# Kernel optimization log

Measured on AMD Instinct MI355X. Metric: run time of the kernel, lower is better.

## Reference

```python
import jax, jax.numpy as jnp
import numpy as np

B, S, E, H = 2, 2048, 1024, 16
D = E // H  # 64 head dim


def _rope_tables(seq_len, d_head, base=10000.0):
    half = d_head // 2
    inv_freq = 1.0 / (base ** (np.arange(0, half, dtype=np.float32) / half))
    t = np.arange(seq_len, dtype=np.float32)
    ang = np.outer(t, inv_freq)  # [S, d_head/2]
    return jnp.asarray(np.cos(ang)), jnp.asarray(np.sin(ang))


def setup_inputs() -> dict:
    key = jax.random.key(0)
    k1, k2, k3 = jax.random.split(key, 3)
    x = jax.random.normal(k1, (B, S, E), dtype=jnp.float32)
    w_qkv = jax.random.normal(k2, (E, 3 * E), dtype=jnp.float32) / np.sqrt(E)
    w_out = jax.random.normal(k3, (E, E), dtype=jnp.float32) / np.sqrt(E)
    freqs_cos, freqs_sin = _rope_tables(S, D)
    return {"x": x, "w_qkv": w_qkv, "w_out": w_out,
            "freqs_cos": freqs_cos, "freqs_sin": freqs_sin}


def _apply_rope(x, cos, sin):
    # x: [B, H, S, D]; cos/sin: [S, D/2] -> broadcast [1, 1, S, D/2]
    xr = x.reshape(*x.shape[:-1], D // 2, 2)
    x0, x1 = xr[..., 0], xr[..., 1]
    c = cos[None, None, :, :]
    s = sin[None, None, :, :]
    out = jnp.stack([x0 * c - x1 * s, x0 * s + x1 * c], axis=-1)
    return out.reshape(x.shape)


def reference(x, w_qkv, w_out, freqs_cos, freqs_sin):
    qkv = x @ w_qkv  # [B, S, 3E]
    q, k, v = jnp.split(qkv, 3, axis=-1)
    def heads(t):
        return t.reshape(B, S, H, D).transpose(0, 2, 1, 3)  # [B, H, S, D]
    q, k, v = heads(q), heads(k), heads(v)
    q = _apply_rope(q, freqs_cos, freqs_sin)
    k = _apply_rope(k, freqs_cos, freqs_sin)
    scale = 1.0 / np.sqrt(D).astype(np.float32)
    scores = jnp.einsum('bhsd,bhtd->bhst', q, k) * scale  # [B, H, S, S]
    causal = jnp.tril(jnp.ones((S, S), dtype=bool))
    scores = jnp.where(causal[None, None], scores, jnp.finfo(scores.dtype).min)
    attn = jax.nn.softmax(scores, axis=-1)
    out = jnp.einsum('bhst,bhtd->bhsd', attn, v)  # [B, H, S, D]
    out = out.transpose(0, 2, 1, 3).reshape(B, S, E)
    return out @ w_out  # dropout is identity in eval mode
```

## Files before the change

### kernel.cpp

```cpp
#include <hip/hip_runtime.h>
#include <cstdint>
#include <cstddef>

typedef unsigned short u16;
typedef __attribute__((ext_vector_type(8))) short bf16x8;
typedef __attribute__((ext_vector_type(8))) unsigned short u16x8;
typedef __attribute__((ext_vector_type(4))) float f32x4;

static constexpr int Bc = 2, Sc = 2048, Ec = 1024, Hc = 16, Dc = 64;

__device__ __forceinline__ float bf2f(u16 v) {
    unsigned u = ((unsigned)v) << 16;
    float f; __builtin_memcpy(&f, &u, 4); return f;
}
__device__ __forceinline__ u16 f2bf(float f) {
    unsigned u; __builtin_memcpy(&u, &f, 4);
    u += 0x7fffu + ((u >> 16) & 1u);
    return (u16)(u >> 16);
}
__device__ __forceinline__ bf16x8 as_bf(u16x8 v) { return __builtin_bit_cast(bf16x8, v); }

__global__ void cast_f32_bf16(const float* __restrict__ in, u16* __restrict__ out, int n) {
    int i = (blockIdx.x * blockDim.x + threadIdx.x) * 4;
    if (i < n) {
        float4 v = *reinterpret_cast<const float4*>(in + i);
        ushort4 o;
        o.x = f2bf(v.x); o.y = f2bf(v.y); o.z = f2bf(v.z); o.w = f2bf(v.w);
        *reinterpret_cast<ushort4*>(out + i) = o;
    }
}

__global__ void transpose_cast(const float* __restrict__ in, u16* __restrict__ out,
                               int R, int C) {
    __shared__ float tile[32][33];
    int tx = threadIdx.x, ty = threadIdx.y;
    int c0 = blockIdx.x * 32, r0 = blockIdx.y * 32;
    tile[ty][tx] = in[(size_t)(r0 + ty) * C + c0 + tx];
    __syncthreads();
    out[(size_t)(c0 + ty) * R + r0 + tx] = f2bf(tile[tx][ty]);
}

template <int OUT_BF16>
__global__ __launch_bounds__(256) void gemm_bt(const u16* __restrict__ A,
                                               const u16* __restrict__ Bt,
                                               void* __restrict__ Cout,
                                               int M, int N, int K) {
    constexpr int BK = 32;
    __shared__ u16 As[128][BK];
    __shared__ u16 Bs[128][BK];
    const int m0 = blockIdx.x * 128, n0 = blockIdx.y * 128;
    const int t = threadIdx.x;
    const int lane = t & 63, w = t >> 6;
    const int wr = w >> 1, wc = w & 1;
    const int l15 = lane & 15, lhi = lane >> 4;
    const int lrow = lane >> 2, lcol = (lane & 3) * 8;

    f32x4 acc[4][4] = {};

    for (int k0 = 0; k0 < K; k0 += BK) {
#pragma unroll
        for (int i = 0; i < 2; i++) {
            const u16* ap = A + (size_t)(m0 + w * 32 + i * 16 + lrow) * K + k0 + lcol;
            __builtin_amdgcn_global_load_lds(
                (const __attribute__((address_space(1))) unsigned int*)ap,
                (__attribute__((address_space(3))) unsigned int*)&As[w * 32 + i * 16][0],
                16, 0, 0);
            const u16* bp = Bt + (size_t)(n0 + w * 32 + i * 16 + lrow) * K + k0 + lcol;
            __builtin_amdgcn_global_load_lds(
                (const __attribute__((address_space(1))) unsigned int*)bp,
                (__attribute__((address_space(3))) unsigned int*)&Bs[w * 32 + i * 16][0],
                16, 0, 0);
        }
        __syncthreads();

        bf16x8 af[4], bfv[4];
#pragma unroll
        for (int i = 0; i < 4; i++)
            af[i] = as_bf(*reinterpret_cast<const u16x8*>(&As[wr * 64 + i * 16 + l15][lhi * 8]));
#pragma unroll
        for (int j = 0; j < 4; j++)
            bfv[j] = as_bf(*reinterpret_cast<const u16x8*>(&Bs[wc * 64 + j * 16 + l15][lhi * 8]));
#pragma unroll
        for (int i = 0; i < 4; i++)
#pragma unroll
            for (int j = 0; j < 4; j++)
                acc[i][j] = __builtin_amdgcn_mfma_f32_16x16x32_bf16(af[i], bfv[j], acc[i][j], 0, 0, 0);
        __syncthreads();
    }

#pragma unroll
    for (int i = 0; i < 4; i++)
#pragma unroll
        for (int j = 0; j < 4; j++)
#pragma unroll
            for (int r = 0; r < 4; r++) {
                int row = m0 + wr * 64 + i * 16 + lhi * 4 + r;
                int col = n0 + wc * 64 + j * 16 + l15;
                float v = acc[i][j][r];
                if (OUT_BF16)
                    ((u16*)Cout)[(size_t)row * N + col] = f2bf(v);
                else
                    ((float*)Cout)[(size_t)row * N + col] = v;
            }
}

__global__ void rope_pack(const u16* __restrict__ qkv,
                          const float* __restrict__ fcos, const float* __restrict__ fsin,
                          u16* __restrict__ Qb, u16* __restrict__ Kb) {
    int g = blockIdx.x * blockDim.x + threadIdx.x;
    int dg = g & 3;
    int h = (g >> 2) & 15;
    int row = g >> 6;
    int b = row >> 11, s = row & 2047;
    const float QS = 0.18033688011f;

    const u16* qp = qkv + (size_t)row * 3072 + h * 64 + dg * 16;
    u16x8 q0 = *reinterpret_cast<const u16x8*>(qp);
    u16x8 q1 = *reinterpret_cast<const u16x8*>(qp + 8);
    u16x8 k0 = *reinterpret_cast<const u16x8*>(qp + 1024);
    u16x8 k1 = *reinterpret_cast<const u16x8*>(qp + 1032);

    const float* cp = fcos + (size_t)s * 32 + dg * 8;
    const float* sp = fsin + (size_t)s * 32 + dg * 8;
    float cs[8], sn[8];
#pragma unroll
    for (int p = 0; p < 8; p++) { cs[p] = cp[p]; sn[p] = sp[p]; }

    u16 qi[16], ki[16], qo[16], ko[16];
#pragma unroll
    for (int j = 0; j < 8; j++) { qi[j] = q0[j]; qi[j + 8] = q1[j]; ki[j] = k0[j]; ki[j + 8] = k1[j]; }
#pragma unroll
    for (int p = 0; p < 8; p++) {
        float x0 = bf2f(qi[2 * p]), x1 = bf2f(qi[2 * p + 1]);
        qo[2 * p]     = f2bf((x0 * cs[p] - x1 * sn[p]) * QS);
        qo[2 * p + 1] = f2bf((x0 * sn[p] + x1 * cs[p]) * QS);
        float y0 = bf2f(ki[2 * p]), y1 = bf2f(ki[2 * p + 1]);
        ko[2 * p]     = f2bf(y0 * cs[p] - y1 * sn[p]);
        ko[2 * p + 1] = f2bf(y0 * sn[p] + y1 * cs[p]);
    }

    size_t dst = ((size_t)(b * 16 + h) * 2048 + s) * 64 + dg * 16;
    u16x8 qa, qb2, ka, kb2;
#pragma unroll
    for (int j = 0; j < 8; j++) { qa[j] = qo[j]; qb2[j] = qo[j + 8]; ka[j] = ko[j]; kb2[j] = ko[j + 8]; }
    *reinterpret_cast<u16x8*>(Qb + dst) = qa;
    *reinterpret_cast<u16x8*>(Qb + dst + 8) = qb2;
    *reinterpret_cast<u16x8*>(Kb + dst) = ka;
    *reinterpret_cast<u16x8*>(Kb + dst + 8) = kb2;
}

__global__ __launch_bounds__(256) void vtrans(const u16* __restrict__ qkv,
                                              u16* __restrict__ VT) {
    __shared__ u16 tile[64][70];
    const int bh = blockIdx.y, b = bh >> 4, h = bh & 15;
    const int s0 = blockIdx.x * 64;
    const int t = threadIdx.x;
    const int si = t >> 2, dc = (t & 3) * 16;
    const u16* src = qkv + (size_t)(b * 2048 + s0 + si) * 3072 + 2048 + h * 64 + dc;
    *reinterpret_cast<u16x8*>(&tile[si][dc])     = *reinterpret_cast<const u16x8*>(src);
    *reinterpret_cast<u16x8*>(&tile[si][dc + 8]) = *reinterpret_cast<const u16x8*>(src + 8);
    __syncthreads();
    const int d = t >> 2, sc = (t & 3) * 16;
    u16x8 v0, v1;
#pragma unroll
    for (int j = 0; j < 8; j++) { v0[j] = tile[sc + j][d]; v1[j] = tile[sc + 8 + j][d]; }
    size_t dst = ((size_t)bh * 64 + d) * 2048 + s0 + sc;
    *reinterpret_cast<u16x8*>(VT + dst)     = v0;
    *reinterpret_cast<u16x8*>(VT + dst + 8) = v1;
}

__global__ __launch_bounds__(256) void attn_fwd5(const u16* __restrict__ Qb,
                                                 const u16* __restrict__ Kb,
                                                 const u16* __restrict__ VTb,
                                                 u16* __restrict__ attn_out) {
    __shared__ u16 Ps[4][32 * 70];
    __shared__ float Om[2][32][64];
    __shared__ float Ol[2][32];

    const int t = threadIdx.x, lane = t & 63, w = t >> 6;
    const int l15 = lane & 15, lhi = lane >> 4;
    const int c = w >> 1;
    const int half = w & 1;

    const int id = blockIdx.x;
    const int bh = (id & 7) + 8 * ((id >> 3) & 3);
    const int kk = 31 - (id >> 5);
    const int qc = 2 * kk + c;
    const int q0 = qc * 32;
    const int b = bh >> 4, h = bh & 15;
    const u16* Kp = Kb + (size_t)bh * (Sc * Dc);
    const u16* Vp = VTb + (size_t)bh * (Sc * Dc);
    u16* PsW = &Ps[w][0];

    bf16x8 qf[2][2];
#pragma unroll
    for (int qa = 0; qa < 2; qa++)
#pragma unroll
        for (int kc = 0; kc < 2; kc++)
            qf[qa][kc] = as_bf(*reinterpret_cast<const u16x8*>(
                Qb + (size_t)bh * (Sc * Dc) + (size_t)(q0 + qa * 16 + l15) * 64 + kc * 32 + lhi * 8));

    u16x8 onesu;
#pragma unroll
    for (int j = 0; j < 8; j++) onesu[j] = 0x3F80;
    const bf16x8 onesf = as_bf(onesu);

    f32x4 o[2][4] = {};
    f32x4 os[2] = {};

    const int ntiles = kk + 1;
    const int nh = (ntiles + 1) >> 1;
    const int kt0 = half ? nh : 0;
    const int kt1 = half ? ntiles : nh;
    const int last = (ntiles - 1) * 64;

    for (int kt = kt0; kt < kt1; kt++) {
        const int t0 = kt * 64;

        f32x4 s[2][4];
        {
            bf16x8 kf[4];
#pragma unroll
            for (int cb = 0; cb < 4; cb++)
                kf[cb] = as_bf(*reinterpret_cast<const u16x8*>(
                    Kp + (size_t)(t0 + cb * 16 + l15) * 64 + lhi * 8));
#pragma unroll
            for (int qa = 0; qa < 2; qa++)
#pragma unroll
                for (int cb = 0; cb < 4; cb++) {
                    f32x4 v = {-14.0f, -14.0f, -14.0f, -14.0f};
                    s[qa][cb] = __builtin_amdgcn_mfma_f32_16x16x32_bf16(qf[qa][0], kf[cb], v, 0, 0, 0);
                }
        }
        {
            bf16x8 kf[4];
#pragma unroll
            for (int cb = 0; cb < 4; cb++)
                kf[cb] = as_bf(*reinterpret_cast<const u16x8*>(
                    Kp + (size_t)(t0 + cb * 16 + l15) * 64 + 32 + lhi * 8));
#pragma unroll
            for (int qa = 0; qa < 2; qa++)
#pragma unroll
                for (int cb = 0; cb < 4; cb++)
                    s[qa][cb] = __builtin_amdgcn_mfma_f32_16x16x32_bf16(qf[qa][1], kf[cb], s[qa][cb], 0, 0, 0);
        }

        if (t0 == last) {
#pragma unroll
            for (int qa = 0; qa < 2; qa++)
#pragma unroll
                for (int cb = 0; cb < 4; cb++) {
                    const int tg = t0 + cb * 16 + l15;
#pragma unroll
                    for (int r = 0; r < 4; r++) {
                        const int qg = q0 + qa * 16 + lhi * 4 + r;
                        if (tg > qg) s[qa][cb][r] = -1e30f;
                    }
                }
        }

#pragma unroll
        for (int qa = 0; qa < 2; qa++)
#pragma unroll
            for (int cb = 0; cb < 4; cb++)
#pragma unroll
                for (int r = 0; r < 4; r++) {
                    float p = __builtin_amdgcn_exp2f(s[qa][cb][r]);
                    unsigned pb; __builtin_memcpy(&pb, &p, 4);
                    PsW[(qa * 16 + lhi * 4 + r) * 70 + cb * 16 + l15] = (u16)(pb >> 16);
                }
        asm volatile("s_waitcnt lgkmcnt(0)" ::: "memory");
        __builtin_amdgcn_sched_barrier(0);

#pragma unroll
        for (int kc = 0; kc < 2; kc++) {
            bf16x8 vf[4];
#pragma unroll
            for (int db = 0; db < 4; db++)
                vf[db] = as_bf(*reinterpret_cast<const u16x8*>(
                    Vp + (size_t)(db * 16 + l15) * 2048 + t0 + kc * 32 + lhi * 8));
#pragma unroll
            for (int qa = 0; qa < 2; qa++) {
                bf16x8 pf = as_bf(*reinterpret_cast<const u16x8*>(
                    &PsW[(qa * 16 + l15) * 70 + kc * 32 + lhi * 8]));
                os[qa] = __builtin_amdgcn_mfma_f32_16x16x32_bf16(pf, onesf, os[qa], 0, 0, 0);
#pragma unroll
                for (int db = 0; db < 4; db++)
                    o[qa][db] = __builtin_amdgcn_mfma_f32_16x16x32_bf16(pf, vf[db], o[qa][db], 0, 0, 0);
            }
        }
    }

    if (half) {
#pragma unroll
        for (int qa = 0; qa < 2; qa++)
#pragma unroll
            for (int r = 0; r < 4; r++) {
                const int row = qa * 16 + lhi * 4 + r;
                if (l15 == 0) Ol[c][row] = os[qa][r];
                f32x4 pk;
#pragma unroll
                for (int db = 0; db < 4; db++) pk[db] = o[qa][db][r];
                *reinterpret_cast<f32x4*>(&Om[c][row][l15 * 4]) = pk;
            }
    }
    __syncthreads();
    if (!half) {
#pragma unroll
        for (int qa = 0; qa < 2; qa++)
#pragma unroll
            for (int r = 0; r < 4; r++) {
                const int row = qa * 16 + lhi * 4 + r;
                const float l = os[qa][r] + Ol[c][row];
                const float inv = 1.0f / l;
                f32x4 pk = *reinterpret_cast<const f32x4*>(&Om[c][row][l15 * 4]);
                const int qg = q0 + row;
                const size_t orow = ((size_t)(b * 2048 + qg)) * 1024 + h * 64;
#pragma unroll
                for (int db = 0; db < 4; db++)
                    attn_out[orow + db * 16 + l15] = f2bf((o[qa][db][r] + pk[db]) * inv);
            }
    }
}

extern "C" void kernel_launch(void* const* d_in, const int* in_sizes, int n_in,
                              void* d_out, int out_size, void* d_ws, size_t ws_size,
                              hipStream_t stream) {
    const float* x     = (const float*)d_in[0];
    const float* w_qkv = (const float*)d_in[1];
    const float* w_out = (const float*)d_in[2];
    const float* fcos  = (const float*)d_in[3];
    const float* fsin  = (const float*)d_in[4];
    float* out = (float*)d_out;

    char* ws = (char*)d_ws;
    u16* xb    = (u16*)(ws);
    u16* wqkvT = (u16*)(ws + 8388608);
    u16* woutT = (u16*)(ws + 14680064);
    u16* qkvb  = (u16*)(ws + 16777216);
    u16* Qb    = (u16*)(ws + 41943040);
    u16* Kb    = (u16*)(ws + 50331648);
    u16* VTb   = (u16*)(ws + 58720256);
    u16* attnb = (u16*)(ws + 67108864);

    cast_f32_bf16<<<4096, 256, 0, stream>>>(x, xb, Bc * Sc * Ec);
    transpose_cast<<<dim3(96, 32), dim3(32, 32), 0, stream>>>(w_qkv, wqkvT, 1024, 3072);
    transpose_cast<<<dim3(32, 32), dim3(32, 32), 0, stream>>>(w_out, woutT, 1024, 1024);
    gemm_bt<1><<<dim3(32, 24), 256, 0, stream>>>(xb, wqkvT, qkvb, 4096, 3072, 1024);
    rope_pack<<<1024, 256, 0, stream>>>(qkvb, fcos, fsin, Qb, Kb);
    vtrans<<<dim3(32, 32), 256, 0, stream>>>(qkvb, VTb);
    attn_fwd5<<<1024, 256, 0, stream>>>(Qb, Kb, VTb, attnb);
    gemm_bt<0><<<dim3(32, 8), 256, 0, stream>>>(attnb, woutT, out, 4096, 1024, 1024);
}
```

Baseline: 230.2 us.

## Balance causal attention work by pairing short and long query chunks per block

Each block now handles a pair of query chunks (63-p and p) whose key-tile counts sum to a constant 33, and splits those 33 tiles across four waves (9,8,8,8). Per-wave partial results are combined with LDS atomics into shared accumulators, and the final normalize-and-store is vectorized. The aim is to remove the per-block load imbalance of causal attention and the tail effect across blocks. In exchange it adds LDS atomic traffic, a zero-init pass, and reloads of the Q fragments for each segment.

Measured after the change: 269.2 us. 1.17x slower.

```diff
diff --git a/kernel.cpp b/kernel.cpp
--- a/kernel.cpp
+++ b/kernel.cpp
@@ -169,7 +169,7 @@
     *reinterpret_cast<u16x8*>(VT + dst + 8) = v1;
 }
 
-__global__ __launch_bounds__(256) void attn_fwd5(const u16* __restrict__ Qb,
+__global__ __launch_bounds__(256) void attn_fwd6(const u16* __restrict__ Qb,
                                                  const u16* __restrict__ Kb,
                                                  const u16* __restrict__ VTb,
                                                  u16* __restrict__ attn_out) {
@@ -179,147 +179,177 @@
 
     const int t = threadIdx.x, lane = t & 63, w = t >> 6;
     const int l15 = lane & 15, lhi = lane >> 4;
-    const int c = w >> 1;
-    const int half = w & 1;
 
     const int id = blockIdx.x;
     const int bh = (id & 7) + 8 * ((id >> 3) & 3);
-    const int kk = 31 - (id >> 5);
-    const int qc = 2 * kk + c;
-    const int q0 = qc * 32;
+    const int p = id >> 5;
     const int b = bh >> 4, h = bh & 15;
+    const u16* Qp = Qb + (size_t)bh * (Sc * Dc);
     const u16* Kp = Kb + (size_t)bh * (Sc * Dc);
     const u16* Vp = VTb + (size_t)bh * (Sc * Dc);
     u16* PsW = &Ps[w][0];
 
-    bf16x8 qf[2][2];
-#pragma unroll
-    for (int qa = 0; qa < 2; qa++)
-#pragma unroll
-        for (int kc = 0; kc < 2; kc++)
-            qf[qa][kc] = as_bf(*reinterpret_cast<const u16x8*>(
-                Qb + (size_t)bh * (Sc * Dc) + (size_t)(q0 + qa * 16 + l15) * 64 + kc * 32 + lhi * 8));
+    for (int i = t; i < 2 * 32 * 64; i += 256) ((float*)Om)[i] = 0.f;
+    if (t < 64) ((float*)Ol)[t] = 0.f;
+    __syncthreads();
 
     u16x8 onesu;
 #pragma unroll
     for (int j = 0; j < 8; j++) onesu[j] = 0x3F80;
     const bf16x8 onesf = as_bf(onesu);
 
-    f32x4 o[2][4] = {};
-    f32x4 os[2] = {};
-
-    const int ntiles = kk + 1;
-    const int nh = (ntiles + 1) >> 1;
-    const int kt0 = half ? nh : 0;
-    const int kt1 = half ? ntiles : nh;
-    const int last = (ntiles - 1) * 64;
-
-    for (int kt = kt0; kt < kt1; kt++) {
-        const int t0 = kt * 64;
-
-        f32x4 s[2][4];
-        {
-            bf16x8 kf[4];
-#pragma unroll
-            for (int cb = 0; cb < 4; cb++)
-                kf[cb] = as_bf(*reinterpret_cast<const u16x8*>(
-                    Kp + (size_t)(t0 + cb * 16 + l15) * 64 + lhi * 8));
+    const int nh = ((63 - p) >> 1) + 1;
+    const int g0 = w ? 9 + (w - 1) * 8 : 0;
+    const int g1 = w ? g0 + 8 : 9;
+
+    for (int seg = 0; seg < 2; seg++) {
+        const int a0 = seg ? (g0 > nh ? g0 : nh) : g0;
+        const int a1 = seg ? g1 : (g1 < nh ? g1 : nh);
+        if (a0 >= a1) continue;
+        const int qc = seg ? p : 63 - p;
+        const int q0 = qc * 32;
+        const int ktoff = seg ? nh : 0;
+        const int ntl = seg ? 33 - nh : nh;
+
+        bf16x8 qf[2][2];
+#pragma unroll
+        for (int qa = 0; qa < 2; qa++)
+#pragma unroll
+            for (int kc = 0; kc < 2; kc++)
+                qf[qa][kc] = as_bf(*reinterpret_cast<const u16x8*>(
+                    Qp + (size_t)(q0 + qa * 16 + l15) * 64 + kc * 32 + lhi * 8));
+
+        f32x4 o[2][4] = {};
+        f32x4 os[2] = {};
+
+        for (int g = a0; g < a1; g++) {
+            const int kt = g - ktoff;
+            const int t0 = kt * 64;
+            const bool diag = (kt == ntl - 1);
+
+            f32x4 s[2][4];
+            {
+                bf16x8 kf[4];
+#pragma unroll
+                for (int cb = 0; cb < 4; cb++)
+                    kf[cb] = as_bf(*reinterpret_cast<const u16x8*>(
+                        Kp + (size_t)(t0 + cb * 16 + l15) * 64 + lhi * 8));
+#pragma unroll
+                for (int qa = 0; qa < 2; qa++)
+#pragma unroll
+                    for (int cb = 0; cb < 4; cb++) {
+                        f32x4 v = {-14.0f, -14.0f, -14.0f, -14.0f};
+                        s[qa][cb] = __builtin_amdgcn_mfma_f32_16x16x32_bf16(qf[qa][0], kf[cb], v, 0, 0, 0);
+                    }
+            }
+            {
+                bf16x8 kf[4];
+#pragma unroll
+                for (int cb = 0; cb < 4; cb++)
+                    kf[cb] = as_bf(*reinterpret_cast<const u16x8*>(
+                        Kp + (size_t)(t0 + cb * 16 + l15) * 64 + 32 + lhi * 8));
+#pragma unroll
+                for (int qa = 0; qa < 2; qa++)
+#pragma unroll
+                    for (int cb = 0; cb < 4; cb++)
+                        s[qa][cb] = __builtin_amdgcn_mfma_f32_16x16x32_bf16(qf[qa][1], kf[cb], s[qa][cb], 0, 0, 0);
+            }
+
+            bf16x8 vf0[4];
+#pragma unroll
+            for (int db = 0; db < 4; db++)
+                vf0[db] = as_bf(*reinterpret_cast<const u16x8*>(
+                    Vp + (size_t)(db * 16 + l15) * 2048 + t0 + lhi * 8));
+
+            if (diag) {
+#pragma unroll
+                for (int qa = 0; qa < 2; qa++)
+#pragma unroll
+                    for (int cb = 0; cb < 4; cb++) {
+                        const int tg = t0 + cb * 16 + l15;
+#pragma unroll
+                        for (int r = 0; r < 4; r++) {
+                            const int qg = q0 + qa * 16 + lhi * 4 + r;
+                            if (tg > qg) s[qa][cb][r] = -1e30f;
+                        }
+                    }
+            }
+
 #pragma unroll
             for (int qa = 0; qa < 2; qa++)
 #pragma unroll
-                for (int cb = 0; cb < 4; cb++) {
-                    f32x4 v = {-14.0f, -14.0f, -14.0f, -14.0f};
-                    s[qa][cb] = __builtin_amdgcn_mfma_f32_16x16x32_bf16(qf[qa][0], kf[cb], v, 0, 0, 0);
-                }
-        }
-        {
-            bf16x8 kf[4];
-#pragma unroll
-            for (int cb = 0; cb < 4; cb++)
-                kf[cb] = as_bf(*reinterpret_cast<const u16x8*>(
-                    Kp + (size_t)(t0 + cb * 16 + l15) * 64 + 32 + lhi * 8));
-#pragma unroll
-            for (int qa = 0; qa < 2; qa++)
-#pragma unroll
                 for (int cb = 0; cb < 4; cb++)
-                    s[qa][cb] = __builtin_amdgcn_mfma_f32_16x16x32_bf16(qf[qa][1], kf[cb], s[qa][cb], 0, 0, 0);
-        }
-
-        if (t0 == last) {
-#pragma unroll
-            for (int qa = 0; qa < 2; qa++)
-#pragma unroll
-                for (int cb = 0; cb < 4; cb++) {
-                    const int tg = t0 + cb * 16 + l15;
 #pragma unroll
                     for (int r = 0; r < 4; r++) {
-                        const int qg = q0 + qa * 16 + lhi * 4 + r;
-                        if (tg > qg) s[qa][cb][r] = -1e30f;
+                        float pv = __builtin_amdgcn_exp2f(s[qa][cb][r]);
+                        unsigned pb; __builtin_memcpy(&pb, &pv, 4);
+                        PsW[(qa * 16 + lhi * 4 + r) * 70 + cb * 16 + l15] = (u16)(pb >> 16);
                     }
-                }
-        }
-
-#pragma unroll
-        for (int qa = 0; qa < 2; qa++)
-#pragma unroll
-            for (int cb = 0; cb < 4; cb++)
-#pragma unroll
-                for (int r = 0; r < 4; r++) {
-                    float p = __builtin_amdgcn_exp2f(s[qa][cb][r]);
-                    unsigned pb; __builtin_memcpy(&pb, &p, 4);
-                    PsW[(qa * 16 + lhi * 4 + r) * 70 + cb * 16 + l15] = (u16)(pb >> 16);
-                }
-        asm volatile("s_waitcnt lgkmcnt(0)" ::: "memory");
-        __builtin_amdgcn_sched_barrier(0);
-
-#pragma unroll
-        for (int kc = 0; kc < 2; kc++) {
-            bf16x8 vf[4];
+            asm volatile("s_waitcnt lgkmcnt(0)" ::: "memory");
+            __builtin_amdgcn_sched_barrier(0);
+
+            bf16x8 vf1[4];
 #pragma unroll
             for (int db = 0; db < 4; db++)
-                vf[db] = as_bf(*reinterpret_cast<const u16x8*>(
-                    Vp + (size_t)(db * 16 + l15) * 2048 + t0 + kc * 32 + lhi * 8));
+                vf1[db] = as_bf(*reinterpret_cast<const u16x8*>(
+                    Vp + (size_t)(db * 16 + l15) * 2048 + t0 + 32 + lhi * 8));
+
 #pragma unroll
             for (int qa = 0; qa < 2; qa++) {
                 bf16x8 pf = as_bf(*reinterpret_cast<const u16x8*>(
-                    &PsW[(qa * 16 + l15) * 70 + kc * 32 + lhi * 8]));
+                    &PsW[(qa * 16 + l15) * 70 + lhi * 8]));
                 os[qa] = __builtin_amdgcn_mfma_f32_16x16x32_bf16(pf, onesf, os[qa], 0, 0, 0);
 #pragma unroll
                 for (int db = 0; db < 4; db++)
-                    o[qa][db] = __builtin_amdgcn_mfma_f32_16x16x32_bf16(pf, vf[db], o[qa][db], 0, 0, 0);
+                    o[qa][db] = __builtin_amdgcn_mfma_f32_16x16x32_bf16(pf, vf0[db], o[qa][db], 0, 0, 0);
+            }
+#pragma unroll
+            for (int qa = 0; qa < 2; qa++) {
+                bf16x8 pf = as_bf(*reinterpret_cast<const u16x8*>(
+                    &PsW[(qa * 16 + l15) * 70 + 32 + lhi * 8]));
+                os[qa] = __builtin_amdgcn_mfma_f32_16x16x32_bf16(pf, onesf, os[qa], 0, 0, 0);
+#pragma unroll
+                for (int db = 0; db < 4; db++)
+                    o[qa][db] = __builtin_amdgcn_mfma_f32_16x16x32_bf16(pf, vf1[db], o[qa][db], 0, 0, 0);
             }
         }
-    }
-
-    if (half) {
+
+        const int ci = seg;
 #pragma unroll
         for (int qa = 0; qa < 2; qa++)
 #pragma unroll
             for (int r = 0; r < 4; r++) {
                 const int row = qa * 16 + lhi * 4 + r;
-                if (l15 == 0) Ol[c][row] = os[qa][r];
-                f32x4 pk;
-#pragma unroll
-                for (int db = 0; db < 4; db++) pk[db] = o[qa][db][r];
-                *reinterpret_cast<f32x4*>(&Om[c][row][l15 * 4]) = pk;
-            }
-    }
+                if (l15 == 0) atomicAdd(&Ol[ci][row], os[qa][r]);
+#pragma unroll
+                for (int db = 0; db < 4; db++)
+                    atomicAdd(&Om[ci][row][db * 16 + l15], o[qa][db][r]);
+            }
+    }
+
     __syncthreads();
-    if (!half) {
-#pragma unroll
-        for (int qa = 0; qa < 2; qa++)
-#pragma unroll
-            for (int r = 0; r < 4; r++) {
-                const int row = qa * 16 + lhi * 4 + r;
-                const float l = os[qa][r] + Ol[c][row];
-                const float inv = 1.0f / l;
-                f32x4 pk = *reinterpret_cast<const f32x4*>(&Om[c][row][l15 * 4]);
-                const int qg = q0 + row;
-                const size_t orow = ((size_t)(b * 2048 + qg)) * 1024 + h * 64;
-#pragma unroll
-                for (int db = 0; db < 4; db++)
-                    attn_out[orow + db * 16 + l15] = f2bf((o[qa][db][r] + pk[db]) * inv);
-            }
+
+    {
+        const int c = w >> 1, sub = w & 1;
+        const int row = sub * 16 + (lane >> 2);
+        const int colq = (lane & 3) * 16;
+        const int qg = (c ? p : 63 - p) * 32 + row;
+        const float inv = 1.0f / Ol[c][row];
+        f32x4 v0 = *reinterpret_cast<const f32x4*>(&Om[c][row][colq]);
+        f32x4 v1 = *reinterpret_cast<const f32x4*>(&Om[c][row][colq + 4]);
+        f32x4 v2 = *reinterpret_cast<const f32x4*>(&Om[c][row][colq + 8]);
+        f32x4 v3 = *reinterpret_cast<const f32x4*>(&Om[c][row][colq + 12]);
+        u16x8 o0, o1;
+#pragma unroll
+        for (int j = 0; j < 4; j++) {
+            o0[j]     = f2bf(v0[j] * inv);
+            o0[j + 4] = f2bf(v1[j] * inv);
+            o1[j]     = f2bf(v2[j] * inv);
+            o1[j + 4] = f2bf(v3[j] * inv);
+        }
+        const size_t obase = ((size_t)(b * 2048 + qg)) * 1024 + h * 64 + colq;
+        *reinterpret_cast<u16x8*>(attn_out + obase)     = o0;
+        *reinterpret_cast<u16x8*>(attn_out + obase + 8) = o1;
     }
 }
 
@@ -349,6 +379,6 @@
     gemm_bt<1><<<dim3(32, 24), 256, 0, stream>>>(xb, wqkvT, qkvb, 4096, 3072, 1024);
     rope_pack<<<1024, 256, 0, stream>>>(qkvb, fcos, fsin, Qb, Kb);
     vtrans<<<dim3(32, 32), 256, 0, stream>>>(qkvb, VTb);
-    attn_fwd5<<<1024, 256, 0, stream>>>(Qb, Kb, VTb, attnb);
+    attn_fwd6<<<1024, 256, 0, stream>>>(Qb, Kb, VTb, attnb);
     gemm_bt<0><<<dim3(32, 8), 256, 0, stream>>>(attnb, woutT, out, 4096, 1024, 1024);
 }
```
